# Optimization experiments

Hardware: AMD Instinct MI355X
Metric: run time of the kernel (lower is better)

The kernel has to match this reference:

```python
import jax, jax.numpy as jnp
import numpy as np

B, H, W, P, DEPTH = 128, 512, 512, 64, 4
EPS = 1e-5


def _std(t):
    # torch.std default: unbiased (ddof=1), over last two dims, keepdim
    m = t.mean(axis=(-2, -1), keepdims=True)
    n = t.shape[-1] * t.shape[-2]
    var = ((t - m) ** 2).sum(axis=(-2, -1), keepdims=True) / (n - 1)
    return jnp.sqrt(var)


def _flat_softmax(t):
    # softmax over all non-batch dims (flatten(1).softmax(1).reshape)
    b = t.shape[0]
    return jax.nn.softmax(t.reshape(b, -1), axis=1).reshape(t.shape)


def setup_inputs() -> dict:
    key = jax.random.key(0)
    ks = jax.random.split(key, 9)
    # xavier-uniform-like scale for [*, fan_in, fan_out] params
    def init(k, shape):
        fan_in, fan_out = shape[-2], shape[-1]
        gain = float(np.sqrt(2.0))  # relu gain
        bound = gain * float(np.sqrt(6.0 / (fan_in + fan_out)))
        return jax.random.uniform(k, shape, jnp.float32, -bound, bound)
    return {
        "x": jax.random.normal(ks[0], (B, H, W), jnp.float32),
        "o_xj": init(ks[1], (DEPTH, W, P)),
        "o_xi": init(ks[2], (DEPTH, H, P)),
        "p_xj": init(ks[3], (DEPTH, H, P)),
        "p_xi": init(ks[4], (DEPTH, W, P)),
        "o_rel_xj": init(ks[5], (DEPTH, W, P)),
        "o_rel_xi": init(ks[6], (DEPTH, H, P)),
        "p_rel_xj": init(ks[7], (DEPTH, P, P)),
        "p_rel_xi": init(ks[8], (DEPTH, P, P)),
    }


def reference(x, o_xj, o_xi, p_xj, p_xi, o_rel_xj, o_rel_xi, p_rel_xj, p_rel_xi):
    # eval-mode forward (dropout inactive)
    b, h, w = x.shape
    p = o_xj.shape[-1]
    depth = o_xj.shape[0]
    scale = (h / p) * (w / p)
    x_mean = x.mean(axis=(-2, -1), keepdims=True) * scale  # [B,1,1]
    x_std = _std(x) * scale                                 # [B,1,1]
    xt = jnp.swapaxes(x, -1, -2)                            # [B,W,H]

    projection = jnp.zeros((b, p, p), jnp.float32)
    for d in range(depth):
        # relevance branches on original orientation
        o_rel_xj_sum = _flat_softmax(x @ o_rel_xj[d]).sum(axis=-2)   # [B,P]
        o_rel_xi_sum = _flat_softmax(xt @ o_rel_xi[d]).sum(axis=-2)  # [B,P]
        # projection branches
        o_t_xj = x @ o_xj[d]                                # [B,H,P]
        o_t_xi = xt @ o_xi[d]                               # [B,W,P]
        p_t_xj = jnp.swapaxes(o_t_xj, -1, -2) @ p_xj[d]     # [B,P,P]
        p_t_xi = jnp.swapaxes(o_t_xi, -1, -2) @ p_xi[d]     # [B,P,P]
        # relevance branches on permuted projection
        p_rel_xj_sum = _flat_softmax(p_t_xj @ p_rel_xj[d]).sum(axis=-2)  # [B,P]
        p_rel_xi_sum = _flat_softmax(p_t_xi @ p_rel_xi[d]).sum(axis=-2)  # [B,P]
        f_j = jnp.sqrt(o_rel_xj_sum / p_rel_xj_sum)         # [B,P]
        f_i = jnp.sqrt(o_rel_xi_sum / p_rel_xi_sum)         # [B,P]
        x_buf = p_t_xj * f_j[..., None] + jnp.swapaxes(p_t_xi * f_i[..., None], -1, -2)
        # renormalize to original (scaled) statistics
        x_buf = (x_buf - x_buf.mean(axis=(-2, -1), keepdims=True)) / (_std(x_buf) + EPS)
        x_buf = x_buf * x_std + x_mean
        projection = projection + x_buf
    return projection
```

## Files before the change

### kernel.cpp

```cpp
#include <hip/hip_runtime.h>
#include <math.h>

typedef __attribute__((ext_vector_type(8))) short short8;
typedef __attribute__((ext_vector_type(4))) short short4v;
typedef __attribute__((ext_vector_type(4))) float f32x4;

#define EPSF 1e-5f

__device__ __forceinline__ short f2bf(float f) {
    union { float f; unsigned u; } v; v.f = f;
    unsigned r = (v.u + 0x7FFFu + ((v.u >> 16) & 1u)) >> 16;
    return (short)r;
}

__device__ __forceinline__ void gload16(const void* g, void* l) {
    __builtin_amdgcn_global_load_lds(
        (const __attribute__((address_space(1))) unsigned int*)g,
        (__attribute__((address_space(3))) unsigned int*)l, 16, 0, 0);
}

__global__ __launch_bounds__(256) void prep_kernel(
    const float* __restrict__ x,
    const float* __restrict__ o_xj, const float* __restrict__ o_xi,
    const float* __restrict__ p_xj, const float* __restrict__ p_xi,
    const float* __restrict__ o_rel_xj, const float* __restrict__ o_rel_xi,
    short* __restrict__ xbf, short* __restrict__ xtbf,
    double* __restrict__ part, short* __restrict__ wcat, short* __restrict__ wpt) {
    int tid = threadIdx.x;
    if (blockIdx.x < 8192) {
        int blk = blockIdx.x;
        int b = blk >> 6, t = blk & 63;
        int tr = (t >> 3) * 64, tc = (t & 7) * 64;
        const float* X = x + (size_t)b * 262144;
        __shared__ short tileR[64][82];
        __shared__ double rs[256], rq[256];

        {
            int r = tid >> 2, cseg = (tid & 3) * 16;
            const float* src = X + (size_t)(tr + r) * 512 + tc + cseg;
            double s = 0.0, sq = 0.0;
            short vals[16];
            #pragma unroll
            for (int q = 0; q < 4; q++) {
                float4 f = *(const float4*)(src + q * 4);
                vals[q * 4 + 0] = f2bf(f.x); vals[q * 4 + 1] = f2bf(f.y);
                vals[q * 4 + 2] = f2bf(f.z); vals[q * 4 + 3] = f2bf(f.w);
                s += (double)f.x + (double)f.y + (double)f.z + (double)f.w;
                sq += (double)f.x * f.x + (double)f.y * f.y + (double)f.z * f.z + (double)f.w * f.w;
            }
            int* tp = (int*)&tileR[r][cseg];
            #pragma unroll
            for (int q = 0; q < 8; q++) tp[q] = ((const int*)vals)[q];
            rs[tid] = s; rq[tid] = sq;
        }
        __syncthreads();
        for (int st = 128; st > 0; st >>= 1) {
            if (tid < st) { rs[tid] += rs[tid + st]; rq[tid] += rq[tid + st]; }
            __syncthreads();
        }
        if (tid == 0) { part[blk * 2] = rs[0]; part[blk * 2 + 1] = rq[0]; }

        int w = tid >> 6, l = tid & 63, li = l & 15, lg = l >> 4;
        #pragma unroll
        for (int q = 0; q < 2; q++) {
            int cc = w * 2 + q;
            int Rl = cc >> 1, ktl = cc & 1;
            const int* sp = (const int*)&tileR[Rl * 16 + li][ktl * 32 + lg * 8];
            int tmp[4];
            #pragma unroll
            for (int j = 0; j < 4; j++) tmp[j] = sp[j];
            size_t chunk = (size_t)(b * 32 + (tr >> 4) + Rl) * 16 + (tc >> 5) + ktl;
            *(short8*)(xbf + chunk * 512 + l * 8) = *(const short8*)tmp;
        }
        #pragma unroll
        for (int q = 0; q < 2; q++) {
            int cc = w * 2 + q;
            int Rl = cc >> 1, ktl = cc & 1;
            int c_loc = Rl * 16 + li;
            int rbase = ktl * 32 + lg * 8;
            short8 v;
            #pragma unroll
            for (int e = 0; e < 8; e++) v[e] = tileR[rbase + e][c_loc];
            size_t chunk = (size_t)(b * 32 + (tc >> 4) + Rl) * 16 + (tr >> 5) + ktl;
            *(short8*)(xtbf + chunk * 512 + l * 8) = v;
        }
    } else {
        int idx = (blockIdx.x - 8192) * 256 + tid;
        if (idx < 65536) {
            int l = idx & 63; int chunk = idx >> 6;
            int kt = chunk & 15, ns = (chunk >> 4) & 7, sd = chunk >> 7;
            int side = sd >> 2, dd = sd & 3;
            int n = ns * 16 + (l & 15);
            int k = kt * 32 + (l >> 4) * 8;
            const float* src = (n < 64) ? (side ? o_rel_xi : o_rel_xj)
                                        : (side ? o_xi : o_xj);
            src += (size_t)dd * 32768 + (n & 63);
            short8 v;
            #pragma unroll
            for (int e = 0; e < 8; e++) v[e] = f2bf(src[(size_t)(k + e) * 64]);
            *(short8*)(wcat + (size_t)chunk * 512 + l * 8) = v;
        } else {
            int j = idx - 65536;
            int l = j & 63; int chunk = j >> 6;
            int nq = chunk & 3, kk = (chunk >> 2) & 3, mt = (chunk >> 4) & 3, sd = chunk >> 6;
            int side = sd >> 2, dd = sd & 3;
            int q = nq * 16 + (l & 15);
            int r = mt * 128 + kk * 32 + (l >> 4) * 8;
            const float* src = (side ? p_xi : p_xj) + (size_t)dd * 32768 + q;
            short8 v;
            #pragma unroll
            for (int e = 0; e < 8; e++) v[e] = f2bf(src[(size_t)(r + e) * 64]);
            *(short8*)(wpt + (size_t)chunk * 512 + l * 8) = v;
        }
    }
}

__global__ __launch_bounds__(256) void stats_p1(const float* __restrict__ x,
                                                double* __restrict__ part) {
    int blk = blockIdx.x;
    const float4* X = (const float4*)(x + (size_t)blk * 65536);
    double s = 0.0, sq = 0.0;
    for (int i = threadIdx.x; i < 16384; i += 256) {
        float4 v = X[i];
        s += (double)v.x + (double)v.y + (double)v.z + (double)v.w;
        sq += (double)v.x * v.x + (double)v.y * v.y + (double)v.z * v.z + (double)v.w * v.w;
    }
    __shared__ double rs[256], rq[256];
    rs[threadIdx.x] = s; rq[threadIdx.x] = sq;
    __syncthreads();
    for (int st = 128; st > 0; st >>= 1) {
        if (threadIdx.x < st) { rs[threadIdx.x] += rs[threadIdx.x + st]; rq[threadIdx.x] += rq[threadIdx.x + st]; }
        __syncthreads();
    }
    if (threadIdx.x == 0) { part[blk * 2] = rs[0]; part[blk * 2 + 1] = rq[0]; }
}

__global__ void stats_p2(const double* __restrict__ part, float* __restrict__ stats, int ppb) {
    int b = threadIdx.x;
    double s = 0.0, sq = 0.0;
    for (int p = 0; p < ppb; p++) { s += part[(b * ppb + p) * 2]; sq += part[(b * ppb + p) * 2 + 1]; }
    double n = 262144.0;
    double mean = s / n;
    double var = (sq - n * mean * mean) / (n - 1.0);
    stats[b * 2 + 0] = (float)(mean * 64.0);
    stats[b * 2 + 1] = (float)(sqrt(var) * 64.0);
}

__global__ __launch_bounds__(256, 4) void main_mfma_kernel(
    const short* __restrict__ xbf, const short* __restrict__ xtbf,
    const short* __restrict__ wcat, const short* __restrict__ wpt,
    float* __restrict__ relsum, float* __restrict__ pt) {
    int blk = blockIdx.x;
    int xcd = blk & 7, rest = blk >> 3;
    int d = rest & 3, side = (rest >> 2) & 1, bhi = rest >> 3;
    int b = bhi * 8 + xcd;
    const short* Xsw = (side ? xtbf : xbf) + (size_t)b * 262144;
    const short* Wc  = wcat + (size_t)(side * 4 + d) * 65536;
    const short* Wp  = wpt + (size_t)(side * 4 + d) * 32768;

    __shared__ __align__(16) char lds[33792];
    short* Xs  = (short*)lds;
    short* Wsh = (short*)(lds + 8192);
    short* Tos = (short*)lds;
    short* Wps = (short*)(lds + 17408);

    int tid = threadIdx.x;
    int w = tid >> 6, l = tid & 63, li = l & 15, lg = l >> 4;
    int wm = w >> 1, wn = w & 1;

    f32x4 zero4 = {0.f, 0.f, 0.f, 0.f};
    f32x4 ptacc[4];
    #pragma unroll
    for (int i = 0; i < 4; i++) ptacc[i] = zero4;
    float esum[4] = {0.f, 0.f, 0.f, 0.f};

    for (int mt = 0; mt < 4; mt++) {
        f32x4 acc[4][4];
        #pragma unroll
        for (int i = 0; i < 4; i++)
            #pragma unroll
            for (int j = 0; j < 4; j++) acc[i][j] = zero4;

        for (int kt = 0; kt < 16; kt++) {
            __syncthreads();
            #pragma unroll
            for (int ii = 0; ii < 4; ii++) {
                int s = w * 4 + ii;
                if (s < 8)
                    gload16(Xsw + ((size_t)((mt * 8 + s) * 16 + kt)) * 512 + l * 8, Xs + s * 512);
                else
                    gload16(Wc + ((size_t)((s - 8) * 16 + kt)) * 512 + l * 8, Wsh + (s - 8) * 512);
            }
            __syncthreads();
            short8 af[4], bfv[4];
            #pragma unroll
            for (int i = 0; i < 4; i++) af[i] = *(const short8*)(Xs + (wm * 4 + i) * 512 + l * 8);
            #pragma unroll
            for (int j = 0; j < 4; j++) bfv[j] = *(const short8*)(Wsh + (wn * 4 + j) * 512 + l * 8);
            #pragma unroll
            for (int i = 0; i < 4; i++)
                #pragma unroll
                for (int j = 0; j < 4; j++)
                    acc[i][j] = __builtin_amdgcn_mfma_f32_16x16x32_bf16(af[i], bfv[j], acc[i][j], 0, 0, 0);
        }

        #pragma unroll
        for (int ii = 0; ii < 4; ii++) {
            int s = w * 4 + ii;
            gload16(Wp + ((size_t)((mt * 4 + (s >> 2)) * 4 + (s & 3))) * 512 + l * 8, Wps + s * 512);
        }
        __syncthreads();

        if (wn == 0) {
            #pragma unroll
            for (int i = 0; i < 4; i++)
                #pragma unroll
                for (int j = 0; j < 4; j++)
                    esum[j] += __expf(acc[i][j][0]) + __expf(acc[i][j][1]) +
                               __expf(acc[i][j][2]) + __expf(acc[i][j][3]);
        } else {
            #pragma unroll
            for (int i = 0; i < 4; i++)
                #pragma unroll
                for (int j = 0; j < 4; j++) {
                    int p = j * 16 + li;
                    int rb = wm * 64 + i * 16 + lg * 4;
                    short4v tv;
                    tv.x = f2bf(acc[i][j][0]); tv.y = f2bf(acc[i][j][1]);
                    tv.z = f2bf(acc[i][j][2]); tv.w = f2bf(acc[i][j][3]);
                    *(short4v*)(Tos + p * 136 + rb) = tv;
                }
        }
        __syncthreads();

        #pragma unroll
        for (int kk = 0; kk < 4; kk++) {
            short8 a = *(const short8*)(Tos + (w * 16 + li) * 136 + kk * 32 + lg * 8);
            #pragma unroll
            for (int nq = 0; nq < 4; nq++) {
                short8 bb = *(const short8*)(Wps + (kk * 4 + nq) * 512 + l * 8);
                ptacc[nq] = __builtin_amdgcn_mfma_f32_16x16x32_bf16(a, bb, ptacc[nq], 0, 0, 0);
            }
        }
    }

    __syncthreads();
    float* red = (float*)lds;
    if (wn == 0) {
        #pragma unroll
        for (int j = 0; j < 4; j++) red[wm * 256 + l * 4 + j] = esum[j];
    }
    __syncthreads();
    size_t base = (size_t)(b * 2 + side) * 4 + d;
    if (tid < 64) {
        float s = 0.f;
        #pragma unroll
        for (int w2 = 0; w2 < 2; w2++)
            #pragma unroll
            for (int g = 0; g < 4; g++)
                s += red[w2 * 256 + (g * 16 + (tid & 15)) * 4 + (tid >> 4)];
        float tot = s;
        #pragma unroll
        for (int off = 1; off < 64; off <<= 1) tot += __shfl_xor(tot, off, 64);
        relsum[base * 64 + tid] = s / tot;
    }
    float* ptout = pt + base * 4096;
    #pragma unroll
    for (int nq = 0; nq < 4; nq++)
        #pragma unroll
        for (int r = 0; r < 4; r++)
            ptout[(size_t)(w * 16 + lg * 4 + r) * 64 + nq * 16 + li] = ptacc[nq][r];
}

__global__ __launch_bounds__(256) void fused_proj_kernel(
    const float* __restrict__ x,
    const float* __restrict__ o_xj, const float* __restrict__ o_xi,
    const float* __restrict__ p_xj, const float* __restrict__ p_xi,
    const float* __restrict__ o_rel_xj, const float* __restrict__ o_rel_xi,
    float* __restrict__ relsum, float* __restrict__ pt)
{
    int blk = blockIdx.x;
    int b = blk >> 3;
    int side = (blk >> 2) & 1;
    int d = blk & 3;

    const float* Wrel = (side ? o_rel_xi : o_rel_xj) + (size_t)d * (512 * 64);
    const float* Wo   = (side ? o_xi     : o_xj)     + (size_t)d * (512 * 64);
    const float* Wp   = (side ? p_xi     : p_xj)     + (size_t)d * (512 * 64);
    const float* X = x + (size_t)b * (512 * 512);

    __shared__ float Xs[16][68];
    __shared__ float Ws[16][128];
    __shared__ float To[64][68];
    __shared__ float Wps[64][68];
    __shared__ float red[16][64];
    __shared__ float cs[64];
    __shared__ float total_s;

    int tid = threadIdx.x;
    int tx = tid & 15;
    int ty = tid >> 4;

    float paccum[4][4];
    #pragma unroll
    for (int i = 0; i < 4; i++)
        #pragma unroll
        for (int j = 0; j < 4; j++) paccum[i][j] = 0.f;
    float esum[8];
    #pragma unroll
    for (int j = 0; j < 8; j++) esum[j] = 0.f;

    for (int r0 = 0; r0 < 512; r0 += 64) {
        float acc[4][8];
        #pragma unroll
        for (int i = 0; i < 4; i++)
            #pragma unroll
            for (int j = 0; j < 8; j++) acc[i][j] = 0.f;

        for (int k0 = 0; k0 < 512; k0 += 16) {
            if (side == 0) {
                int kk = tid & 15, r = tid >> 4;
                #pragma unroll
                for (int it = 0; it < 4; it++, r += 16)
                    Xs[kk][r] = X[(size_t)(r0 + r) * 512 + (k0 + kk)];
            } else {
                int r = tid & 63, kk = tid >> 6;
                #pragma unroll
                for (int it = 0; it < 4; it++, kk += 4)
                    Xs[kk][r] = X[(size_t)(k0 + kk) * 512 + (r0 + r)];
            }
            {
                int c = tid & 127, kk = tid >> 7;
                const float* Wsrc = (c < 64) ? (Wrel + c) : (Wo + (c - 64));
                #pragma unroll
                for (int it = 0; it < 8; it++, kk += 2)
                    Ws[kk][c] = Wsrc[(size_t)(k0 + kk) * 64];
            }
            __syncthreads();
            #pragma unroll
            for (int kk = 0; kk < 16; kk++) {
                float4 a  = *(const float4*)&Xs[kk][ty * 4];
                float4 b0 = *(const float4*)&Ws[kk][tx * 8];
                float4 b1 = *(const float4*)&Ws[kk][tx * 8 + 4];
                float av[4] = {a.x, a.y, a.z, a.w};
                float bv[8] = {b0.x, b0.y, b0.z, b0.w, b1.x, b1.y, b1.z, b1.w};
                #pragma unroll
                for (int i = 0; i < 4; i++)
                    #pragma unroll
                    for (int j = 0; j < 8; j++)
                        acc[i][j] = fmaf(av[i], bv[j], acc[i][j]);
            }
            __syncthreads();
        }

        if (tx < 8) {
            #pragma unroll
            for (int i = 0; i < 4; i++)
                #pragma unroll
                for (int j = 0; j < 8; j++)
                    esum[j] += expf(acc[i][j]);
        } else {
            #pragma unroll
            for (int i = 0; i < 4; i++) {
                float4 v0 = make_float4(acc[i][0], acc[i][1], acc[i][2], acc[i][3]);
                float4 v1 = make_float4(acc[i][4], acc[i][5], acc[i][6], acc[i][7]);
                *(float4*)&To[ty * 4 + i][(tx - 8) * 8]     = v0;
                *(float4*)&To[ty * 4 + i][(tx - 8) * 8 + 4] = v1;
            }
        }
        {
            int q = tid & 63, r = tid >> 6;
            #pragma unroll
            for (int it = 0; it < 16; it++, r += 4)
                Wps[r][q] = Wp[(size_t)(r0 + r) * 64 + q];
        }
        __syncthreads();
        for (int r = 0; r < 64; r++) {
            float4 aa = *(const float4*)&To[r][ty * 4];
            float4 bb = *(const float4*)&Wps[r][tx * 4];
            float av[4] = {aa.x, aa.y, aa.z, aa.w};
            float bv[4] = {bb.x, bb.y, bb.z, bb.w};
            #pragma unroll
            for (int i = 0; i < 4; i++)
                #pragma unroll
                for (int j = 0; j < 4; j++)
                    paccum[i][j] = fmaf(av[i], bv[j], paccum[i][j]);
        }
        __syncthreads();
    }

    if (tx < 8) {
        #pragma unroll
        for (int j = 0; j < 8; j++) red[ty][tx * 8 + j] = esum[j];
    }
    __syncthreads();
    if (tid < 64) {
        float s = 0.f;
        for (int t = 0; t < 16; t++) s += red[t][tid];
        cs[tid] = s;
    }
    __syncthreads();
    if (tid == 0) {
        float tot = 0.f;
        for (int i = 0; i < 64; i++) tot += cs[i];
        total_s = tot;
    }
    __syncthreads();
    size_t base = (size_t)(b * 2 + side) * 4 + d;
    if (tid < 64) relsum[base * 64 + tid] = cs[tid] / total_s;

    float* ptout = pt + base * 4096;
    #pragma unroll
    for (int i = 0; i < 4; i++)
        #pragma unroll
        for (int j = 0; j < 4; j++)
            ptout[(size_t)(ty * 4 + i) * 64 + tx * 4 + j] = paccum[i][j];
}

__global__ __launch_bounds__(256) void finalize2_kernel(
    const float* __restrict__ relsum, const float* __restrict__ pt,
    const float* __restrict__ p_rel_xj, const float* __restrict__ p_rel_xi,
    const double* __restrict__ part, const float* __restrict__ stats, int ppb,
    float* __restrict__ out)
{
    int blk = blockIdx.x;
    int b = blk >> 2, d = blk & 3;
    int tid = threadIdx.x, tx = tid & 15, ty = tid >> 4;
    __shared__ __align__(16) float Ptj[64][68], Pti[64][68], Wr[64][68];
    __shared__ float red[16][64];
    __shared__ float fj[64], fi[64];
    __shared__ float rs[256], rq[256];
    __shared__ float bc[1];
    __shared__ float sstat[2];

    if (ppb > 0) {
        if (tid < 64) {
            double s = part[(size_t)(b * 64 + tid) * 2];
            double sq = part[(size_t)(b * 64 + tid) * 2 + 1];
            #pragma unroll
            for (int off = 1; off < 64; off <<= 1) {
                s += __shfl_xor(s, off, 64);
                sq += __shfl_xor(sq, off, 64);
            }
            if (tid == 0) {
                double n = 262144.0;
                double mean = s / n;
                double var = (sq - n * mean * mean) / (n - 1.0);
                sstat[0] = (float)(mean * 64.0);
                sstat[1] = (float)(sqrt(var) * 64.0);
            }
        }
    } else if (tid == 0) {
        sstat[0] = stats[b * 2 + 0];
        sstat[1] = stats[b * 2 + 1];
    }

    const float* ptj = pt + ((size_t)(b * 2 + 0) * 4 + d) * 4096;
    const float* pti = pt + ((size_t)(b * 2 + 1) * 4 + d) * 4096;
    for (int it = 0; it < 16; it++) {
        int idx = tid + it * 256;
        Ptj[idx >> 6][idx & 63] = ptj[idx];
        Pti[idx >> 6][idx & 63] = pti[idx];
    }
    __syncthreads();
    float x_mean = sstat[0];
    float x_std  = sstat[1];

    for (int s = 0; s < 2; s++) {
        const float* prel = (s == 0) ? (p_rel_xj + (size_t)d * 4096)
                                     : (p_rel_xi + (size_t)d * 4096);
        for (int it = 0; it < 16; it++) {
            int idx = tid + it * 256;
            Wr[idx >> 6][idx & 63] = prel[idx];
        }
        __syncthreads();
        const float (*Pt)[68] = (s == 0) ? Ptj : Pti;
        float q[4][4];
        #pragma unroll
        for (int i = 0; i < 4; i++)
            #pragma unroll
            for (int j = 0; j < 4; j++) q[i][j] = 0.f;
        for (int r = 0; r < 64; r++) {
            float4 bv = *(const float4*)&Wr[r][tx * 4];
            #pragma unroll
            for (int i = 0; i < 4; i++) {
                float a = Pt[ty * 4 + i][r];
                q[i][0] = fmaf(a, bv.x, q[i][0]);
                q[i][1] = fmaf(a, bv.y, q[i][1]);
                q[i][2] = fmaf(a, bv.z, q[i][2]);
                q[i][3] = fmaf(a, bv.w, q[i][3]);
            }
        }
        float cpart[4];
        #pragma unroll
        for (int j = 0; j < 4; j++)
            cpart[j] = __expf(q[0][j]) + __expf(q[1][j]) + __expf(q[2][j]) + __expf(q[3][j]);
        #pragma unroll
        for (int j = 0; j < 4; j++) red[ty][tx * 4 + j] = cpart[j];
        __syncthreads();
        float* ftgt = (s == 0) ? fj : fi;
        if (tid < 64) {
            float cssum = 0.f;
            for (int t = 0; t < 16; t++) cssum += red[t][tid];
            ftgt[tid] = cssum;
        }
        __syncthreads();
        if (tid == 0) {
            float tot = 0.f;
            for (int i = 0; i < 64; i++) tot += ftgt[i];
            bc[0] = tot;
        }
        __syncthreads();
        if (tid < 64) {
            float prel_sum = ftgt[tid] / bc[0];
            float orel = relsum[((size_t)(b * 2 + s) * 4 + d) * 64 + tid];
            ftgt[tid] = sqrtf(orel / prel_sum);
        }
        __syncthreads();
    }

    float v[4][4];
    float psum = 0.f, psq = 0.f;
    #pragma unroll
    for (int i = 0; i < 4; i++) {
        int r = ty * 4 + i;
        #pragma unroll
        for (int j = 0; j < 4; j++) {
            int c = tx * 4 + j;
            float val = Ptj[r][c] * fj[r] + Pti[c][r] * fi[c];
            v[i][j] = val; psum += val; psq += val * val;
        }
    }
    rs[tid] = psum; rq[tid] = psq;
    __syncthreads();
    for (int st = 128; st > 0; st >>= 1) {
        if (tid < st) { rs[tid] += rs[tid + st]; rq[tid] += rq[tid + st]; }
        __syncthreads();
    }
    float mean = rs[0] / 4096.f;
    float var = (rq[0] - 4096.f * mean * mean) / 4095.f;
    float inv = 1.0f / (sqrtf(var) + EPSF);
    float* ob = out + (size_t)b * 4096;
    #pragma unroll
    for (int i = 0; i < 4; i++)
        #pragma unroll
        for (int j = 0; j < 4; j++)
            atomicAdd(&ob[(size_t)(ty * 4 + i) * 64 + tx * 4 + j],
                      (v[i][j] - mean) * inv * x_std + x_mean);
}

extern "C" void kernel_launch(void* const* d_in, const int* in_sizes, int n_in,
                              void* d_out, int out_size, void* d_ws, size_t ws_size,
                              hipStream_t stream) {
    const float* x        = (const float*)d_in[0];
    const float* o_xj     = (const float*)d_in[1];
    const float* o_xi     = (const float*)d_in[2];
    const float* p_xj     = (const float*)d_in[3];
    const float* p_xi     = (const float*)d_in[4];
    const float* o_rel_xj = (const float*)d_in[5];
    const float* o_rel_xi = (const float*)d_in[6];
    const float* p_rel_xj = (const float*)d_in[7];
    const float* p_rel_xi = (const float*)d_in[8];
    float* out = (float*)d_out;

    char* ws = (char*)d_ws;
    float*  stats  = (float*)(ws + 0);
    float*  relsum = (float*)(ws + 1024);
    float*  pt     = (float*)(ws + 263168);
    double* spartF = (double*)(ws + 17040384);
    short*  xbf    = (short*)(ws + 17171456);
    short*  xtbf   = (short*)(ws + 84280320);
    short*  wcat   = (short*)(ws + 151389184);
    short*  wptb   = (short*)(ws + 152437760);
    double* spartS = (double*)(ws + 17040384);

    hipMemsetAsync(d_out, 0, (size_t)out_size * sizeof(float), stream);

    const size_t FAST_NEED = 152962048;
    if (ws_size >= FAST_NEED) {
        prep_kernel<<<8576, 256, 0, stream>>>(x, o_xj, o_xi, p_xj, p_xi,
                                              o_rel_xj, o_rel_xi,
                                              xbf, xtbf, spartF, wcat, wptb);
        main_mfma_kernel<<<1024, 256, 0, stream>>>(xbf, xtbf, wcat, wptb, relsum, pt);
        finalize2_kernel<<<512, 256, 0, stream>>>(relsum, pt, p_rel_xj, p_rel_xi,
                                                  spartF, stats, 64, out);
    } else {
        if (ws_size >= 17171456) {
            stats_p1<<<512, 256, 0, stream>>>(x, spartS);
            stats_p2<<<1, 128, 0, stream>>>(spartS, stats, 4);
        } else {
            double* sp = (double*)(ws + 263168);
            stats_p1<<<512, 256, 0, stream>>>(x, sp);
            stats_p2<<<1, 128, 0, stream>>>(sp, stats, 4);
        }
        fused_proj_kernel<<<1024, 256, 0, stream>>>(x, o_xj, o_xi, p_xj, p_xi,
                                                    o_rel_xj, o_rel_xi, relsum, pt);
        finalize2_kernel<<<512, 256, 0, stream>>>(relsum, pt, p_rel_xj, p_rel_xi,
                                                  (const double*)nullptr, stats, 0, out);
    }
}
```

Before: 343.6 us.

## Restructure prep kernel around 16-row fp32 strips loaded directly into LDS

Each prep block now handles a full 16x512 row strip of x (4096 blocks instead of 8192 64x64 tiles). The strip is loaded with global_load_lds async copies into a 32KB fp32 LDS tile, and bf16 conversion happens on read. The block sum reduction now uses wave shuffles instead of an LDS tree with many barriers. The goal is fewer barriers, more efficient global loads and fewer partials per batch (32 instead of 64), paid for with a larger LDS footprint that may limit occupancy and strided transposed LDS reads.

```diff
diff --git a/kernel.cpp b/kernel.cpp
--- a/kernel.cpp
+++ b/kernel.cpp
@@ -27,65 +27,67 @@
     short* __restrict__ xbf, short* __restrict__ xtbf,
     double* __restrict__ part, short* __restrict__ wcat, short* __restrict__ wpt) {
     int tid = threadIdx.x;
-    if (blockIdx.x < 8192) {
+    if (blockIdx.x < 4096) {
         int blk = blockIdx.x;
-        int b = blk >> 6, t = blk & 63;
-        int tr = (t >> 3) * 64, tc = (t & 7) * 64;
-        const float* X = x + (size_t)b * 262144;
-        __shared__ short tileR[64][82];
-        __shared__ double rs[256], rq[256];
-
-        {
-            int r = tid >> 2, cseg = (tid & 3) * 16;
-            const float* src = X + (size_t)(tr + r) * 512 + tc + cseg;
-            double s = 0.0, sq = 0.0;
-            short vals[16];
-            #pragma unroll
-            for (int q = 0; q < 4; q++) {
-                float4 f = *(const float4*)(src + q * 4);
-                vals[q * 4 + 0] = f2bf(f.x); vals[q * 4 + 1] = f2bf(f.y);
-                vals[q * 4 + 2] = f2bf(f.z); vals[q * 4 + 3] = f2bf(f.w);
-                s += (double)f.x + (double)f.y + (double)f.z + (double)f.w;
-                sq += (double)f.x * f.x + (double)f.y * f.y + (double)f.z * f.z + (double)f.w * f.w;
-            }
-            int* tp = (int*)&tileR[r][cseg];
-            #pragma unroll
-            for (int q = 0; q < 8; q++) tp[q] = ((const int*)vals)[q];
-            rs[tid] = s; rq[tid] = sq;
-        }
-        __syncthreads();
-        for (int st = 128; st > 0; st >>= 1) {
-            if (tid < st) { rs[tid] += rs[tid + st]; rq[tid] += rq[tid + st]; }
-            __syncthreads();
-        }
-        if (tid == 0) { part[blk * 2] = rs[0]; part[blk * 2 + 1] = rq[0]; }
-
+        int b = blk >> 5, R = blk & 31;
+        const float* X = x + (size_t)b * 262144 + (size_t)R * 16 * 512;
+        __shared__ __align__(16) float tile[16 * 512];
+        __shared__ double wsum[4][2];
         int w = tid >> 6, l = tid & 63, li = l & 15, lg = l >> 4;
-        #pragma unroll
-        for (int q = 0; q < 2; q++) {
-            int cc = w * 2 + q;
-            int Rl = cc >> 1, ktl = cc & 1;
-            const int* sp = (const int*)&tileR[Rl * 16 + li][ktl * 32 + lg * 8];
-            int tmp[4];
-            #pragma unroll
-            for (int j = 0; j < 4; j++) tmp[j] = sp[j];
-            size_t chunk = (size_t)(b * 32 + (tr >> 4) + Rl) * 16 + (tc >> 5) + ktl;
-            *(short8*)(xbf + chunk * 512 + l * 8) = *(const short8*)tmp;
-        }
-        #pragma unroll
-        for (int q = 0; q < 2; q++) {
-            int cc = w * 2 + q;
-            int Rl = cc >> 1, ktl = cc & 1;
-            int c_loc = Rl * 16 + li;
-            int rbase = ktl * 32 + lg * 8;
-            short8 v;
-            #pragma unroll
-            for (int e = 0; e < 8; e++) v[e] = tileR[rbase + e][c_loc];
-            size_t chunk = (size_t)(b * 32 + (tc >> 4) + Rl) * 16 + (tr >> 5) + ktl;
-            *(short8*)(xtbf + chunk * 512 + l * 8) = v;
+
+        #pragma unroll
+        for (int ii = 0; ii < 8; ii++) {
+            int s = w * 8 + ii;
+            gload16(X + s * 256 + l * 4, tile + s * 256);
+        }
+        __syncthreads();
+
+        double s = 0.0, sq = 0.0;
+        #pragma unroll
+        for (int q = 0; q < 4; q++) {
+            int kt = w * 4 + q;
+            const float* p0 = tile + li * 512 + kt * 32 + lg * 8;
+            float4 f0 = *(const float4*)p0;
+            float4 f1 = *(const float4*)(p0 + 4);
+            short v[8];
+            v[0] = f2bf(f0.x); v[1] = f2bf(f0.y); v[2] = f2bf(f0.z); v[3] = f2bf(f0.w);
+            v[4] = f2bf(f1.x); v[5] = f2bf(f1.y); v[6] = f2bf(f1.z); v[7] = f2bf(f1.w);
+            s += (double)f0.x + (double)f0.y + (double)f0.z + (double)f0.w
+               + (double)f1.x + (double)f1.y + (double)f1.z + (double)f1.w;
+            sq += (double)f0.x * f0.x + (double)f0.y * f0.y + (double)f0.z * f0.z + (double)f0.w * f0.w
+                + (double)f1.x * f1.x + (double)f1.y * f1.y + (double)f1.z * f1.z + (double)f1.w * f1.w;
+            size_t chunk = (size_t)((b * 32 + R) * 16 + kt);
+            *(short8*)(xbf + chunk * 512 + l * 8) = *(const short8*)v;
+        }
+
+        int base_lg = (R & 1) * 2;
+        int kt2 = R >> 1;
+        int lh = l & 31, li2 = lh & 15, lgo = lh >> 4;
+        #pragma unroll
+        for (int q = 0; q < 4; q++) {
+            int p = w * 8 + q * 2 + (l >> 5);
+            short v[8];
+            #pragma unroll
+            for (int e = 0; e < 8; e++)
+                v[e] = f2bf(tile[(lgo * 8 + e) * 512 + p * 16 + li2]);
+            size_t chunk = (size_t)((b * 32 + p) * 16 + kt2);
+            *(short8*)(xtbf + chunk * 512 + (base_lg + lgo) * 128 + li2 * 8) = *(const short8*)v;
+        }
+
+        #pragma unroll
+        for (int off = 1; off < 64; off <<= 1) {
+            s += __shfl_xor(s, off, 64);
+            sq += __shfl_xor(sq, off, 64);
+        }
+        if (l == 0) { wsum[w][0] = s; wsum[w][1] = sq; }
+        __syncthreads();
+        if (tid == 0) {
+            double ts = wsum[0][0] + wsum[1][0] + wsum[2][0] + wsum[3][0];
+            double tq = wsum[0][1] + wsum[1][1] + wsum[2][1] + wsum[3][1];
+            part[blk * 2] = ts; part[blk * 2 + 1] = tq;
         }
     } else {
-        int idx = (blockIdx.x - 8192) * 256 + tid;
+        int idx = (blockIdx.x - 4096) * 256 + tid;
         if (idx < 65536) {
             int l = idx & 63; int chunk = idx >> 6;
             int kt = chunk & 15, ns = (chunk >> 4) & 7, sd = chunk >> 7;
@@ -434,11 +436,10 @@
     __shared__ float sstat[2];
 
     if (ppb > 0) {
-        if (tid < 64) {
-            double s = part[(size_t)(b * 64 + tid) * 2];
-            double sq = part[(size_t)(b * 64 + tid) * 2 + 1];
-            #pragma unroll
-            for (int off = 1; off < 64; off <<= 1) {
+        if (tid < ppb) {
+            double s = part[(size_t)(b * ppb + tid) * 2];
+            double sq = part[(size_t)(b * ppb + tid) * 2 + 1];
+            for (int off = 1; off < ppb; off <<= 1) {
                 s += __shfl_xor(s, off, 64);
                 sq += __shfl_xor(sq, off, 64);
             }
@@ -578,12 +579,12 @@
 
     const size_t FAST_NEED = 152962048;
     if (ws_size >= FAST_NEED) {
-        prep_kernel<<<8576, 256, 0, stream>>>(x, o_xj, o_xi, p_xj, p_xi,
+        prep_kernel<<<4480, 256, 0, stream>>>(x, o_xj, o_xi, p_xj, p_xi,
                                               o_rel_xj, o_rel_xi,
                                               xbf, xtbf, spartF, wcat, wptb);
         main_mfma_kernel<<<1024, 256, 0, stream>>>(xbf, xtbf, wcat, wptb, relsum, pt);
         finalize2_kernel<<<512, 256, 0, stream>>>(relsum, pt, p_rel_xj, p_rel_xi,
-                                                  spartF, stats, 64, out);
+                                                  spartF, stats, 32, out);
     } else {
         if (ws_size >= 17171456) {
             stats_p1<<<512, 256, 0, stream>>>(x, spartS);
```

Result: no change. 338.9 us (-1.4%).
